# Optimization experiments

Hardware: AMD Instinct MI355X
Metric: run time of the kernel (lower is better)

The kernel has to match this reference:

```python
import jax, jax.numpy as jnp
import numpy as np

B, S, H, R = 4, 4096, 768, 242
HK = H // 3  # k/v/attn-output feature dim (256)
THETA = 10000.0


def _rope_table(seq_len, dim, theta=THETA):
    # Reproduces LlamaRotaryEmbedding.forward: returns [seq_len, dim] = cat(sin, cos)
    pos = jnp.arange(seq_len, dtype=jnp.float32)
    freqs = theta ** (-jnp.arange(0, dim, 2, dtype=jnp.float32) / dim)  # [dim/2]
    ang = pos[:, None] * freqs[None, :]  # [S, dim/2]
    return jnp.concatenate([jnp.sin(ang), jnp.cos(ang)], axis=-1)  # [S, dim]


def setup_inputs() -> dict:
    key = jax.random.key(0)
    ks = jax.random.split(key, 9)
    init = lambda k, shape: (jax.random.normal(k, shape, dtype=jnp.float32) * 0.02)
    return {
        "x": jax.random.normal(ks[0], (B, S, H), dtype=jnp.float32),
        # torch nn.Linear weights have shape [out_features, in_features]; y = x @ W.T
        "q_low": init(ks[1], (R, H)),  "q_high": init(ks[2], (H, R)),
        "k_low": init(ks[3], (R, H)),  "k_high": init(ks[4], (HK, R)),
        "v_low": init(ks[5], (R, H)),  "v_high": init(ks[6], (HK, R)),
        "o_low": init(ks[7], (R, HK)), "o_high": init(ks[8], (H, R)),
    }


def reference(x, q_low, q_high, k_low, k_high, v_low, v_high, o_low, o_high):
    b, s, h = x.shape
    # NOTE: in the original module, rope_emb(q) / rope_emb(k) discard the projected
    # q/k values and return the same [S, H] sin/cos position table, so q_proj/k_proj
    # are dead code (XLA will DCE them). We keep only the live computation.
    v = (x @ v_low.T) @ v_high.T  # [B, S, HK] factorized v projection
    t = _rope_table(s, h)         # q = k = t, shape [S, H]
    attn = jax.nn.softmax(t @ t.T, axis=-1)  # [S, S], input-independent
    ctx = jnp.einsum('st,btd->bsd', attn, v)  # [B, S, HK]
    return (ctx @ o_low.T) @ o_high.T         # [B, S, H]
```

## Files before the change

### kernel.cpp

```cpp
#include <hip/hip_runtime.h>
#include <hip/hip_bf16.h>


typedef __bf16 bf16x8 __attribute__((ext_vector_type(8)));
typedef __bf16 bf16x4 __attribute__((ext_vector_type(4)));
typedef float  f32x4  __attribute__((ext_vector_type(4)));

#define GLD16(g, l) __builtin_amdgcn_global_load_lds(                         \
    (const __attribute__((address_space(1))) void*)(g),                       \
    (__attribute__((address_space(3))) void*)(l), 16, 0, 0)


__global__ __launch_bounds__(256) void prep_ptvlt(const float* __restrict__ vh,
                                                  const float* __restrict__ ol,
                                                  const float* __restrict__ vl,
                                                  __bf16* __restrict__ pt,
                                                  __bf16* __restrict__ vlt) {
    if (blockIdx.x < 242) {
        int j = blockIdx.x, i = threadIdx.x;
        float s = 0.f;
        if (i < 242) {
#pragma unroll 32
            for (int k = 0; k < 256; ++k)
                s += vh[k * 242 + i] * ol[j * 256 + k];
        }
        pt[j * 256 + i] = (__bf16)s;
    } else {
        int n = (blockIdx.x - 242) * 256 + threadIdx.x;
        int i = n >> 8, r = n & 255;
        vlt[n] = (r < 242) ? (__bf16)vl[r * 768 + i] : (__bf16)0.f;
    }
}

__global__ __launch_bounds__(256) void prep_q(const __bf16* __restrict__ pt,
                                              const float* __restrict__ oh,
                                              __bf16* __restrict__ qb) {
    int j = blockIdx.x, r = threadIdx.x;
    float s = 0.f;
#pragma unroll 32
    for (int k = 0; k < 242; ++k)
        s += (float)pt[k * 256 + r] * oh[j * 242 + k];
    qb[j * 256 + r] = (__bf16)s;
}

__global__ __launch_bounds__(256) void gemm_nt_w(const __bf16* __restrict__ A,
                                                 const __bf16* __restrict__ Bt,
                                                 __bf16* __restrict__ C) {
    __shared__ alignas(16) __bf16 lA[8 * 64 * 32];
    __shared__ alignas(16) __bf16 lB[8 * 64 * 32];

    const int tid  = threadIdx.x;
    const int wave = tid >> 6, lane = tid & 63;
    const int quad = lane >> 4, l16 = lane & 15;
    const int wm = (wave >> 1) * 32, wn = (wave & 1) * 32;

    const __bf16* Ab = A + (long)blockIdx.x * 64 * 256;
    const __bf16* Bb = Bt + (long)blockIdx.y * 64 * 256;

    const int sr = wave * 16 + (lane >> 2);
    const int sc = (lane & 3) * 8;
#pragma unroll
    for (int kc = 0; kc < 8; ++kc) {
        GLD16(Ab + sr * 256 + kc * 32 + sc, &lA[kc * 2048 + wave * 512]);
        GLD16(Bb + sr * 256 + kc * 32 + sc, &lB[kc * 2048 + wave * 512]);
    }
    __syncthreads();

    f32x4 acc[2][2] = {};
#pragma unroll
    for (int kc = 0; kc < 8; ++kc) {
        bf16x8 af[2], bfr[2];
#pragma unroll
        for (int i = 0; i < 2; ++i) {
            af[i]  = *(const bf16x8*)&lA[kc * 2048 + (wm + i * 16 + l16) * 32 + quad * 8];
            bfr[i] = *(const bf16x8*)&lB[kc * 2048 + (wn + i * 16 + l16) * 32 + quad * 8];
        }
#pragma unroll
        for (int mi = 0; mi < 2; ++mi)
#pragma unroll
            for (int ni = 0; ni < 2; ++ni)
                acc[mi][ni] = __builtin_amdgcn_mfma_f32_16x16x32_bf16(
                    af[mi], bfr[ni], acc[mi][ni], 0, 0, 0);
    }

    const int rb = blockIdx.x * 64 + wm + quad * 4;
    const int ib = blockIdx.y * 64 + wn + l16;
#pragma unroll
    for (int mi = 0; mi < 2; ++mi)
#pragma unroll
        for (int ni = 0; ni < 2; ++ni) {
            const int i  = ib + ni * 16;
            const int kc = i >> 5, qi = (i >> 3) & 3, e = i & 7;
#pragma unroll
            for (int j = 0; j < 4; ++j) {
                const int r = rb + mi * 16 + j;
                const int g = r >> 4, lr = r & 15;
                C[((g * 24 + kc) * 64 + qi * 16 + lr) * 8 + e] =
                    (__bf16)acc[mi][ni][j];
            }
        }
}

__global__ __launch_bounds__(1024, 4) void gemm_xw(const float* __restrict__ A,
                                                   const __bf16* __restrict__ Bt,
                                                   float* __restrict__ C) {
    __shared__ alignas(16) __bf16 lA[2][64 * 256];

    const int tid  = threadIdx.x;
    const int wave = tid >> 6, lane = tid & 63;
    const int quad = lane >> 4, l16 = lane & 15;

    const int mt = blockIdx.x;
    const float* Ab = A + (long)mt * 64 * 768;

    const int srow = tid >> 4;
    const float* ga = Ab + srow * 768 + (tid & 15) * 16;
    const int sw  = (srow & 7) << 4;
    const int wb0 = srow * 512 + (((tid & 15) * 32)      ^ sw);
    const int wb1 = srow * 512 + (((tid & 15) * 32 + 16) ^ sw);
    const int rsw = (l16 & 7) << 4;

    const __bf16* Bw = Bt + (long)wave * 3 * 24 * 512 + lane * 8;

    f32x4 acc[3][4] = {};

    {
        f32x4 s0 = *(const f32x4*)(ga);
        f32x4 s1 = *(const f32x4*)(ga + 4);
        f32x4 s2 = *(const f32x4*)(ga + 8);
        f32x4 s3 = *(const f32x4*)(ga + 12);
        bf16x8 h0 = { (__bf16)s0[0], (__bf16)s0[1], (__bf16)s0[2], (__bf16)s0[3],
                      (__bf16)s1[0], (__bf16)s1[1], (__bf16)s1[2], (__bf16)s1[3] };
        bf16x8 h1 = { (__bf16)s2[0], (__bf16)s2[1], (__bf16)s2[2], (__bf16)s2[3],
                      (__bf16)s3[0], (__bf16)s3[1], (__bf16)s3[2], (__bf16)s3[3] };
        *(bf16x8*)((char*)&lA[0][0] + wb0) = h0;
        *(bf16x8*)((char*)&lA[0][0] + wb1) = h1;
    }
    __syncthreads();

#pragma unroll
    for (int c = 0; c < 3; ++c) {
        f32x4 s0, s1, s2, s3;
        if (c < 2) {
            const float* gn = ga + (c + 1) * 256;
            s0 = *(const f32x4*)(gn);
            s1 = *(const f32x4*)(gn + 4);
            s2 = *(const f32x4*)(gn + 8);
            s3 = *(const f32x4*)(gn + 12);
        }

        const char* lb = (const char*)&lA[c & 1][0];
#pragma unroll
        for (int kf = 0; kf < 8; ++kf) {
            bf16x8 b[3];
#pragma unroll
            for (int g = 0; g < 3; ++g)
                b[g] = *(const bf16x8*)(Bw + ((g * 24 + c * 8 + kf) << 9));
            bf16x8 af[4];
#pragma unroll
            for (int m = 0; m < 4; ++m) {
                const int off = (m * 16 + l16) * 512 +
                                ((kf * 64 + quad * 16) ^ rsw);
                af[m] = *(const bf16x8*)(lb + off);
            }
#pragma unroll
            for (int g = 0; g < 3; ++g)
#pragma unroll
                for (int m = 0; m < 4; ++m)
                    acc[g][m] = __builtin_amdgcn_mfma_f32_16x16x32_bf16(
                        af[m], b[g], acc[g][m], 0, 0, 0);
        }

        if (c < 2) {
            bf16x8 h0 = { (__bf16)s0[0], (__bf16)s0[1], (__bf16)s0[2], (__bf16)s0[3],
                          (__bf16)s1[0], (__bf16)s1[1], (__bf16)s1[2], (__bf16)s1[3] };
            bf16x8 h1 = { (__bf16)s2[0], (__bf16)s2[1], (__bf16)s2[2], (__bf16)s2[3],
                          (__bf16)s3[0], (__bf16)s3[1], (__bf16)s3[2], (__bf16)s3[3] };
            char* wp = (char*)&lA[(c + 1) & 1][0];
            *(bf16x8*)(wp + wb0) = h0;
            *(bf16x8*)(wp + wb1) = h1;
            __syncthreads();
        }
    }

    const long rb = (long)mt * 64 + quad * 4;
    const int  cb = wave * 48 + l16;
#pragma unroll
    for (int g = 0; g < 3; ++g)
#pragma unroll
        for (int m = 0; m < 4; ++m)
#pragma unroll
            for (int j = 0; j < 4; ++j)
                C[(rb + m * 16 + j) * 768 + cb + g * 16] = acc[g][m][j];
}


extern "C" void kernel_launch(void* const* d_in, const int* in_sizes, int n_in,
                              void* d_out, int out_size, void* d_ws, size_t ws_size,
                              hipStream_t stream) {
    const float* x      = (const float*)d_in[0];
    const float* v_low  = (const float*)d_in[5];
    const float* v_high = (const float*)d_in[6];
    const float* o_low  = (const float*)d_in[7];
    const float* o_high = (const float*)d_in[8];
    float* out = (float*)d_out;

    char* ws = (char*)d_ws;
    __bf16* pt  = (__bf16*)(ws + 0);
    __bf16* qb  = (__bf16*)(ws + 262144);
    __bf16* vlt = (__bf16*)(ws + 655360);
    __bf16* wtb = (__bf16*)(ws + 1048576);

    prep_ptvlt<<<1010, 256, 0, stream>>>(v_high, o_low, v_low, pt, vlt);
    prep_q    <<<768,  256, 0, stream>>>(pt, o_high, qb);

    gemm_nt_w<<<dim3(12, 12), 256, 0, stream>>>(qb, vlt, wtb);

    gemm_xw<<<256, 1024, 0, stream>>>(x, wtb, out);
}
```

Baseline: 145.9 us.

## Restructure x@W GEMM: keep full A tile in LDS, loop output groups outermost

The gemm_xw kernel now stages the whole 64x768 bf16 A tile in 96KB of dynamic LDS, no longer double-buffering 256-column chunks. It loops over the three output column groups outermost and stores each group's accumulators right after computing it, so global stores overlap the next group's MFMA work. This cuts live B fragments from three to one per step. The cost is re-reading A from LDS three times, a larger LDS footprint that may lower occupancy, and dropping the launch-bounds occupancy hint.

New measurement: 150.2 us. 3.0% more time.

```diff
diff --git a/kernel.cpp b/kernel.cpp
--- a/kernel.cpp
+++ b/kernel.cpp
@@ -3,7 +3,6 @@
 
 
 typedef __bf16 bf16x8 __attribute__((ext_vector_type(8)));
-typedef __bf16 bf16x4 __attribute__((ext_vector_type(4)));
 typedef float  f32x4  __attribute__((ext_vector_type(4)));
 
 #define GLD16(g, l) __builtin_amdgcn_global_load_lds(                         \
@@ -101,10 +100,10 @@
         }
 }
 
-__global__ __launch_bounds__(1024, 4) void gemm_xw(const float* __restrict__ A,
-                                                   const __bf16* __restrict__ Bt,
-                                                   float* __restrict__ C) {
-    __shared__ alignas(16) __bf16 lA[2][64 * 256];
+__global__ __launch_bounds__(1024) void gemm_xw(const float* __restrict__ A,
+                                                const __bf16* __restrict__ Bt,
+                                                float* __restrict__ C) {
+    extern __shared__ __bf16 lA[];
 
     const int tid  = threadIdx.x;
     const int wave = tid >> 6, lane = tid & 63;
@@ -113,11 +112,11 @@
     const int mt = blockIdx.x;
     const float* Ab = A + (long)mt * 64 * 768;
 
-    const int srow = tid >> 4;
-    const float* ga = Ab + srow * 768 + (tid & 15) * 16;
+    const int srow = tid >> 4, tcol = tid & 15;
+    const float* ga = Ab + srow * 768 + tcol * 16;
     const int sw  = (srow & 7) << 4;
-    const int wb0 = srow * 512 + (((tid & 15) * 32)      ^ sw);
-    const int wb1 = srow * 512 + (((tid & 15) * 32 + 16) ^ sw);
+    const int wb0 = srow * 512 + ((tcol * 32)      ^ sw);
+    const int wb1 = srow * 512 + ((tcol * 32 + 16) ^ sw);
     const int rsw = (l16 & 7) << 4;
 
     const __bf16* Bw = Bt + (long)wave * 3 * 24 * 512 + lane * 8;
@@ -133,65 +132,62 @@
                       (__bf16)s1[0], (__bf16)s1[1], (__bf16)s1[2], (__bf16)s1[3] };
         bf16x8 h1 = { (__bf16)s2[0], (__bf16)s2[1], (__bf16)s2[2], (__bf16)s2[3],
                       (__bf16)s3[0], (__bf16)s3[1], (__bf16)s3[2], (__bf16)s3[3] };
-        *(bf16x8*)((char*)&lA[0][0] + wb0) = h0;
-        *(bf16x8*)((char*)&lA[0][0] + wb1) = h1;
+        *(bf16x8*)((char*)lA + wb0) = h0;
+        *(bf16x8*)((char*)lA + wb1) = h1;
     }
     __syncthreads();
 
-#pragma unroll
-    for (int c = 0; c < 3; ++c) {
-        f32x4 s0, s1, s2, s3;
-        if (c < 2) {
-            const float* gn = ga + (c + 1) * 256;
-            s0 = *(const f32x4*)(gn);
-            s1 = *(const f32x4*)(gn + 4);
-            s2 = *(const f32x4*)(gn + 8);
-            s3 = *(const f32x4*)(gn + 12);
-        }
-
-        const char* lb = (const char*)&lA[c & 1][0];
-#pragma unroll
-        for (int kf = 0; kf < 8; ++kf) {
-            bf16x8 b[3];
-#pragma unroll
-            for (int g = 0; g < 3; ++g)
-                b[g] = *(const bf16x8*)(Bw + ((g * 24 + c * 8 + kf) << 9));
-            bf16x8 af[4];
-#pragma unroll
-            for (int m = 0; m < 4; ++m) {
-                const int off = (m * 16 + l16) * 512 +
-                                ((kf * 64 + quad * 16) ^ rsw);
-                af[m] = *(const bf16x8*)(lb + off);
-            }
-#pragma unroll
-            for (int g = 0; g < 3; ++g)
+    f32x4 t0, t1, t2, t3;
+
+#pragma unroll
+    for (int g = 0; g < 3; ++g) {
+#pragma unroll
+        for (int c = 0; c < 3; ++c) {
+            if (g == 0 && c < 2) {
+                const float* gn = ga + (c + 1) * 256;
+                t0 = *(const f32x4*)(gn);
+                t1 = *(const f32x4*)(gn + 4);
+                t2 = *(const f32x4*)(gn + 8);
+                t3 = *(const f32x4*)(gn + 12);
+            }
+
+            const char* lb = (const char*)lA + c * 32768;
+#pragma unroll
+            for (int kf = 0; kf < 8; ++kf) {
+                bf16x8 b = *(const bf16x8*)(Bw + ((g * 24 + c * 8 + kf) << 9));
+                bf16x8 af[4];
+#pragma unroll
+                for (int m = 0; m < 4; ++m) {
+                    const int off = (m * 16 + l16) * 512 +
+                                    ((kf * 64 + quad * 16) ^ rsw);
+                    af[m] = *(const bf16x8*)(lb + off);
+                }
 #pragma unroll
                 for (int m = 0; m < 4; ++m)
                     acc[g][m] = __builtin_amdgcn_mfma_f32_16x16x32_bf16(
-                        af[m], b[g], acc[g][m], 0, 0, 0);
-        }
-
-        if (c < 2) {
-            bf16x8 h0 = { (__bf16)s0[0], (__bf16)s0[1], (__bf16)s0[2], (__bf16)s0[3],
-                          (__bf16)s1[0], (__bf16)s1[1], (__bf16)s1[2], (__bf16)s1[3] };
-            bf16x8 h1 = { (__bf16)s2[0], (__bf16)s2[1], (__bf16)s2[2], (__bf16)s2[3],
-                          (__bf16)s3[0], (__bf16)s3[1], (__bf16)s3[2], (__bf16)s3[3] };
-            char* wp = (char*)&lA[(c + 1) & 1][0];
-            *(bf16x8*)(wp + wb0) = h0;
-            *(bf16x8*)(wp + wb1) = h1;
-            __syncthreads();
-        }
-    }
-
-    const long rb = (long)mt * 64 + quad * 4;
-    const int  cb = wave * 48 + l16;
-#pragma unroll
-    for (int g = 0; g < 3; ++g)
+                        af[m], b, acc[g][m], 0, 0, 0);
+            }
+
+            if (g == 0 && c < 2) {
+                bf16x8 h0 = { (__bf16)t0[0], (__bf16)t0[1], (__bf16)t0[2], (__bf16)t0[3],
+                              (__bf16)t1[0], (__bf16)t1[1], (__bf16)t1[2], (__bf16)t1[3] };
+                bf16x8 h1 = { (__bf16)t2[0], (__bf16)t2[1], (__bf16)t2[2], (__bf16)t2[3],
+                              (__bf16)t3[0], (__bf16)t3[1], (__bf16)t3[2], (__bf16)t3[3] };
+                char* wp = (char*)lA + (c + 1) * 32768;
+                *(bf16x8*)(wp + wb0) = h0;
+                *(bf16x8*)(wp + wb1) = h1;
+                __syncthreads();
+            }
+        }
+
+        const long rb = (long)mt * 64 + quad * 4;
+        const int  cb = wave * 48 + g * 16 + l16;
 #pragma unroll
         for (int m = 0; m < 4; ++m)
 #pragma unroll
             for (int j = 0; j < 4; ++j)
-                C[(rb + m * 16 + j) * 768 + cb + g * 16] = acc[g][m][j];
+                C[(rb + m * 16 + j) * 768 + cb] = acc[g][m][j];
+    }
 }
 
 
@@ -211,10 +207,17 @@
     __bf16* vlt = (__bf16*)(ws + 655360);
     __bf16* wtb = (__bf16*)(ws + 1048576);
 
+    static bool attr_done = false;
+    if (!attr_done) {
+        hipFuncSetAttribute(reinterpret_cast<const void*>(gemm_xw),
+                            hipFuncAttributeMaxDynamicSharedMemorySize, 98304);
+        attr_done = true;
+    }
+
     prep_ptvlt<<<1010, 256, 0, stream>>>(v_high, o_low, v_low, pt, vlt);
     prep_q    <<<768,  256, 0, stream>>>(pt, o_high, qb);
 
     gemm_nt_w<<<dim3(12, 12), 256, 0, stream>>>(qb, vlt, wtb);
 
-    gemm_xw<<<256, 1024, 0, stream>>>(x, wtb, out);
-}
+    gemm_xw<<<256, 1024, 98304, stream>>>(x, wtb, out);
+}
```
